# Kernel optimization log

Measured on AMD Instinct MI355X. Metric: run time of the kernel, lower is better.

## Reference

```python
import jax, jax.numpy as jnp
import numpy as np

N_NODES = 50000
N_EDGES = 800000
IN_C, HID_C, OUT_C = 256, 256, 128


def gcn_conv(x, W, b, row, col, n_nodes):
    """PyG GCNConv: linear transform, symmetric-normalized aggregation, bias.
    row/col already include self-loops. Messages flow row -> col."""
    h = x @ W  # [N, out]
    deg = jax.ops.segment_sum(jnp.ones_like(col, dtype=h.dtype), col, num_segments=n_nodes)
    d_inv_sqrt = jnp.where(deg > 0, jax.lax.rsqrt(jnp.maximum(deg, 1e-12)), 0.0)
    norm = d_inv_sqrt[row] * d_inv_sqrt[col]  # [E]
    msg = h[row] * norm[:, None]              # gather + scale, [E, out]
    out = jax.ops.segment_sum(msg, col, num_segments=n_nodes)  # scatter-add
    return out + b


def setup_inputs() -> dict:
    key = jax.random.key(0)
    k_x, k_e, k_w1, k_w2 = jax.random.split(key, 4)
    x = jax.random.normal(k_x, (N_NODES, IN_C), dtype=jnp.float32)
    edge_index = jax.random.randint(k_e, (2, N_EDGES), 0, N_NODES, dtype=jnp.int64)
    # Glorot-style init for GCN weights, zeros bias (PyG default)
    s1 = float(np.sqrt(6.0 / (IN_C + HID_C)))
    s2 = float(np.sqrt(6.0 / (HID_C + OUT_C)))
    W1 = jax.random.uniform(k_w1, (IN_C, HID_C), dtype=jnp.float32, minval=-s1, maxval=s1)
    b1 = jnp.zeros((HID_C,), dtype=jnp.float32)
    W2 = jax.random.uniform(k_w2, (HID_C, OUT_C), dtype=jnp.float32, minval=-s2, maxval=s2)
    b2 = jnp.zeros((OUT_C,), dtype=jnp.float32)
    return {"x": x, "edge_index": edge_index, "W1": W1, "b1": b1, "W2": W2, "b2": b2}


def reference(x, edge_index, W1, b1, W2, b2):
    n = x.shape[0]
    # add self-loops (PyG GCNConv default add_self_loops=True)
    loops = jnp.arange(n, dtype=edge_index.dtype)
    row = jnp.concatenate([edge_index[0], loops])
    col = jnp.concatenate([edge_index[1], loops])
    h = gcn_conv(x, W1, b1, row, col, n)
    h = jax.nn.relu(h)  # dropout p=0.0 -> identity
    out = gcn_conv(h, W2, b2, row, col, n)
    return out
```

## Files before the change

kernel.cpp:

```cpp
#include <hip/hip_runtime.h>

#define NN 50000
#define NE 800000
#define IN_C 256
#define HID_C 256
#define OUT_C 128

typedef unsigned short u16;
typedef __attribute__((ext_vector_type(8))) short short8;
typedef __attribute__((ext_vector_type(8))) unsigned short ushort8;
typedef __attribute__((ext_vector_type(4))) float f32x4;

__device__ __forceinline__ u16 f2b(float f) {
  unsigned int u = __float_as_uint(f);
  return (u16)((u + 0x7FFFu + ((u >> 16) & 1u)) >> 16);
}
__device__ __forceinline__ float b2f(u16 s) {
  return __uint_as_float(((unsigned int)s) << 16);
}


__global__ __launch_bounds__(256) void convw_zero(const float* __restrict__ W1,
                                                  const float* __restrict__ W2,
                                                  u16* __restrict__ W1t,
                                                  u16* __restrict__ W2t,
                                                  int* __restrict__ cnt) {
  int b = blockIdx.x;
  if (b < 256) {
    int id = b * 256 + threadIdx.x;
    if (id < 256 * 256) {
      int n = id >> 8, k = id & 255;
      W1t[id] = f2b(W1[k * 256 + n]);
    }
    if (id < 128 * 256) {
      int n = id >> 8, k = id & 255;
      W2t[id] = f2b(W2[k * 128 + n]);
    }
  } else {
    int i = (b - 256) * 256 + threadIdx.x;
    if (i < NN) cnt[i] = 0;
  }
}


__global__ __launch_bounds__(256) void hist_kernel(const int* __restrict__ col,
                                                   int* __restrict__ cnt, int E) {
  int e = blockIdx.x * blockDim.x + threadIdx.x;
  if (e < E) atomicAdd(&cnt[col[e]], 1);
}

__global__ __launch_bounds__(256) void scan1_kernel(const int* __restrict__ cnt,
                                                    int* __restrict__ bsum, int n) {
  __shared__ int ws[4];
  int i = blockIdx.x * 256 + threadIdx.x;
  int lane = threadIdx.x & 63, wid = threadIdx.x >> 6;
  int v = (i < n) ? cnt[i] : 0;
#pragma unroll
  for (int off = 32; off > 0; off >>= 1) v += __shfl_down(v, off, 64);
  if (lane == 0) ws[wid] = v;
  __syncthreads();
  if (threadIdx.x == 0) bsum[blockIdx.x] = ws[0] + ws[1] + ws[2] + ws[3];
}

__global__ __launch_bounds__(256) void scan2_kernel(const int* __restrict__ bsum,
                                                    int* __restrict__ boff,
                                                    int* __restrict__ row_off,
                                                    int nb, int n) {
  __shared__ int wsum[4], wpre[5];
  int lane = threadIdx.x & 63, wid = threadIdx.x >> 6;
  int v = (threadIdx.x < nb) ? bsum[threadIdx.x] : 0;
  int s = v;
#pragma unroll
  for (int off = 1; off < 64; off <<= 1) {
    int t = __shfl_up(s, off, 64);
    if (lane >= off) s += t;
  }
  if (lane == 63) wsum[wid] = s;
  __syncthreads();
  if (threadIdx.x == 0) {
    int acc = 0;
#pragma unroll
    for (int w = 0; w < 4; ++w) { wpre[w] = acc; acc += wsum[w]; }
    wpre[4] = acc;
  }
  __syncthreads();
  if (threadIdx.x < nb) boff[threadIdx.x] = wpre[wid] + (s - v);
  if (threadIdx.x == 0) row_off[n] = wpre[4];
}

__global__ __launch_bounds__(256) void scan3_kernel(const int* __restrict__ cnt,
                                                    const int* __restrict__ boff,
                                                    int* __restrict__ row_off,
                                                    int* __restrict__ cursor,
                                                    float* __restrict__ dinv, int n) {
  __shared__ int wsum[4], wpre[4];
  int i = blockIdx.x * 256 + threadIdx.x;
  int lane = threadIdx.x & 63, wid = threadIdx.x >> 6;
  int v = (i < n) ? cnt[i] : 0;
  int s = v;
#pragma unroll
  for (int off = 1; off < 64; off <<= 1) {
    int t = __shfl_up(s, off, 64);
    if (lane >= off) s += t;
  }
  if (lane == 63) wsum[wid] = s;
  __syncthreads();
  if (threadIdx.x == 0) {
    int acc = 0;
#pragma unroll
    for (int w = 0; w < 4; ++w) { wpre[w] = acc; acc += wsum[w]; }
  }
  __syncthreads();
  if (i < n) {
    int off = boff[blockIdx.x] + wpre[wid] + (s - v);
    row_off[i] = off;
    cursor[i] = off;
    dinv[i] = rsqrtf((float)(v + 1));
  }
}


template <bool A_IS_F32>
__device__ __forceinline__ void gemm_body(const void* __restrict__ Ap,
                                          const u16* __restrict__ Bt,
                                          const float* __restrict__ dscale,
                                          u16* __restrict__ C, int M, int N,
                                          int bx, int by,
                                          u16 (&Asl)[2][5120], u16 (&Bsl)[2][5120]) {
  const int tid = threadIdx.x;
  const int row0 = by * 128;
  const int col0 = bx * 128;

  f32x4 acc[4][4] = {};

  const int seg = tid & 7;
  const int rb = tid >> 3;
  const int wave = tid >> 6, lane = tid & 63;
  const int wm = wave >> 1, wn = wave & 1;
  const int qr = lane & 15, quad = lane >> 4;

  float4 aF[4];
  ushort4 aU[4];
  ushort4 bR[4];

  auto load_tiles = [&](int k0) {
    if constexpr (A_IS_F32) {
      const float* A = (const float*)Ap;
#pragma unroll
      for (int i = 0; i < 4; ++i) {
        int gr = row0 + rb + i * 32;
        aF[i] = (gr < M) ? *(const float4*)&A[(size_t)gr * 256 + k0 + seg * 4]
                         : make_float4(0.f, 0.f, 0.f, 0.f);
      }
    } else {
      const u16* A = (const u16*)Ap;
#pragma unroll
      for (int i = 0; i < 4; ++i) {
        int gr = row0 + rb + i * 32;
        aU[i] = (gr < M) ? *(const ushort4*)&A[(size_t)gr * 256 + k0 + seg * 4]
                         : make_ushort4(0, 0, 0, 0);
      }
    }
#pragma unroll
    for (int i = 0; i < 4; ++i) {
      int n = rb + i * 32;
      bR[i] = *(const ushort4*)&Bt[(size_t)(col0 + n) * 256 + k0 + seg * 4];
    }
  };

  auto write_lds = [&](int buf) {
#pragma unroll
    for (int i = 0; i < 4; ++i) {
      int r = rb + i * 32;
      ushort4 u;
      if constexpr (A_IS_F32) {
        u.x = f2b(aF[i].x); u.y = f2b(aF[i].y);
        u.z = f2b(aF[i].z); u.w = f2b(aF[i].w);
      } else {
        u = aU[i];
      }
      *(ushort4*)&Asl[buf][r * 40 + seg * 4] = u;
      *(ushort4*)&Bsl[buf][r * 40 + seg * 4] = bR[i];
    }
  };

  load_tiles(0);
  write_lds(0);
  __syncthreads();

#pragma unroll
  for (int it = 0; it < 8; ++it) {
    const int cur = it & 1;
    if (it < 7) load_tiles((it + 1) * 32);

    short8 afr[4], bfr[4];
#pragma unroll
    for (int mt = 0; mt < 4; ++mt)
      afr[mt] = *(const short8*)&Asl[cur][(wm * 64 + mt * 16 + qr) * 40 + quad * 8];
#pragma unroll
    for (int nt = 0; nt < 4; ++nt)
      bfr[nt] = *(const short8*)&Bsl[cur][(wn * 64 + nt * 16 + qr) * 40 + quad * 8];
#pragma unroll
    for (int mt = 0; mt < 4; ++mt)
#pragma unroll
      for (int nt = 0; nt < 4; ++nt)
        acc[mt][nt] = __builtin_amdgcn_mfma_f32_16x16x32_bf16(afr[mt], bfr[nt], acc[mt][nt], 0, 0, 0);

    if (it < 7) {
      write_lds(1 - cur);
      __syncthreads();
    }
  }

#pragma unroll
  for (int mt = 0; mt < 4; ++mt) {
#pragma unroll
    for (int i = 0; i < 4; ++i) {
      int gr = row0 + wm * 64 + mt * 16 + quad * 4 + i;
      if (gr < M) {
        float sc = dscale[gr];
#pragma unroll
        for (int nt = 0; nt < 4; ++nt) {
          int gc = col0 + wn * 64 + nt * 16 + qr;
          C[(size_t)gr * N + gc] = f2b(acc[mt][nt][i] * sc);
        }
      }
    }
  }
}

template <bool A_IS_F32>
__global__ __launch_bounds__(256) void gemm_mfma(const void* __restrict__ Ap,
                                                 const u16* __restrict__ Bt,
                                                 const float* __restrict__ dscale,
                                                 u16* __restrict__ C, int M, int N) {
  __shared__ u16 Asl[2][5120];
  __shared__ u16 Bsl[2][5120];
  gemm_body<A_IS_F32>(Ap, Bt, dscale, C, M, N, blockIdx.x, blockIdx.y, Asl, Bsl);
}

__global__ __launch_bounds__(256) void gemm1_scatter(const float* __restrict__ x,
                                                     const u16* __restrict__ W1t,
                                                     const float* __restrict__ dinv,
                                                     u16* __restrict__ Hb, int M, int N,
                                                     int ngb,
                                                     const int* __restrict__ row,
                                                     const int* __restrict__ col,
                                                     int* __restrict__ cursor,
                                                     int* __restrict__ csr, int E) {
  __shared__ u16 Asl[2][5120];
  __shared__ u16 Bsl[2][5120];
  int b = blockIdx.x;
  if (b < ngb) {
    gemm_body<true>(x, W1t, dinv, Hb, M, N, b & 1, b >> 1, Asl, Bsl);
  } else {
    int e = (b - ngb) * 256 + threadIdx.x;
    if (e < E) {
      int c = col[e];
      int p = atomicAdd(&cursor[c], 1);
      csr[p] = row[e];
    }
  }
}


__global__ __launch_bounds__(256) void agg256_bf(const u16* __restrict__ h,
                                                 const int* __restrict__ row_off,
                                                 const int* __restrict__ csr,
                                                 const float* __restrict__ dinv,
                                                 const float* __restrict__ bias,
                                                 u16* __restrict__ out, int n) {
  int wave = threadIdx.x >> 6;
  int lane = threadIdx.x & 63;
  int half = lane >> 5;
  int sl = lane & 31;
  int v = blockIdx.x * 8 + wave * 2 + half;
  if (v >= n) return;
  int beg = row_off[v], end = row_off[v + 1];
  float a[8] = {};
  int e = beg;
  for (; e < end && (e & 3); ++e) {
    int s0 = csr[e];
    ushort8 g0 = *(const ushort8*)&h[(size_t)s0 * 256 + sl * 8];
#pragma unroll
    for (int i = 0; i < 8; ++i) a[i] += b2f((u16)g0[i]);
  }
  for (; e + 7 < end; e += 8) {
    int4 i0 = *(const int4*)&csr[e];
    int4 i1 = *(const int4*)&csr[e + 4];
    int s[8] = {i0.x, i0.y, i0.z, i0.w, i1.x, i1.y, i1.z, i1.w};
    ushort8 g[8];
#pragma unroll
    for (int j = 0; j < 8; ++j)
      g[j] = *(const ushort8*)&h[(size_t)s[j] * 256 + sl * 8];
#pragma unroll
    for (int j = 0; j < 8; ++j)
#pragma unroll
      for (int i = 0; i < 8; ++i) a[i] += b2f((u16)g[j][i]);
  }
  for (; e < end; ++e) {
    int s0 = csr[e];
    ushort8 g0 = *(const ushort8*)&h[(size_t)s0 * 256 + sl * 8];
#pragma unroll
    for (int i = 0; i < 8; ++i) a[i] += b2f((u16)g0[i]);
  }
  ushort8 hs = *(const ushort8*)&h[(size_t)v * 256 + sl * 8];
#pragma unroll
  for (int i = 0; i < 8; ++i) a[i] += b2f((u16)hs[i]);
  float dv = dinv[v];
  float4 bv0 = *(const float4*)&bias[sl * 8];
  float4 bv1 = *(const float4*)&bias[sl * 8 + 4];
  float bb[8] = {bv0.x, bv0.y, bv0.z, bv0.w, bv1.x, bv1.y, bv1.z, bv1.w};
  ushort8 o;
#pragma unroll
  for (int i = 0; i < 8; ++i) {
    float r = fmaxf(a[i] * dv + bb[i], 0.f);
    o[i] = (short)f2b(r);
  }
  *(ushort8*)&out[(size_t)v * 256 + sl * 8] = o;
}

__global__ __launch_bounds__(256) void agg128_bf(const u16* __restrict__ h,
                                                 const int* __restrict__ row_off,
                                                 const int* __restrict__ csr,
                                                 const float* __restrict__ dinv,
                                                 const float* __restrict__ bias,
                                                 float* __restrict__ out, int n) {
  int wave = threadIdx.x >> 6;
  int lane = threadIdx.x & 63;
  int quarter = lane >> 4;
  int sl = lane & 15;
  int v = blockIdx.x * 16 + wave * 4 + quarter;
  if (v >= n) return;
  int beg = row_off[v], end = row_off[v + 1];
  float a[8] = {};
  int e = beg;
  for (; e < end && (e & 3); ++e) {
    int s0 = csr[e];
    ushort8 g0 = *(const ushort8*)&h[(size_t)s0 * 128 + sl * 8];
#pragma unroll
    for (int i = 0; i < 8; ++i) a[i] += b2f((u16)g0[i]);
  }
  for (; e + 7 < end; e += 8) {
    int4 i0 = *(const int4*)&csr[e];
    int4 i1 = *(const int4*)&csr[e + 4];
    int s[8] = {i0.x, i0.y, i0.z, i0.w, i1.x, i1.y, i1.z, i1.w};
    ushort8 g[8];
#pragma unroll
    for (int j = 0; j < 8; ++j)
      g[j] = *(const ushort8*)&h[(size_t)s[j] * 128 + sl * 8];
#pragma unroll
    for (int j = 0; j < 8; ++j)
#pragma unroll
      for (int i = 0; i < 8; ++i) a[i] += b2f((u16)g[j][i]);
  }
  for (; e < end; ++e) {
    int s0 = csr[e];
    ushort8 g0 = *(const ushort8*)&h[(size_t)s0 * 128 + sl * 8];
#pragma unroll
    for (int i = 0; i < 8; ++i) a[i] += b2f((u16)g0[i]);
  }
  ushort8 hs = *(const ushort8*)&h[(size_t)v * 128 + sl * 8];
#pragma unroll
  for (int i = 0; i < 8; ++i) a[i] += b2f((u16)hs[i]);
  float dv = dinv[v];
  float4 bv0 = *(const float4*)&bias[sl * 8];
  float4 bv1 = *(const float4*)&bias[sl * 8 + 4];
  float bb[8] = {bv0.x, bv0.y, bv0.z, bv0.w, bv1.x, bv1.y, bv1.z, bv1.w};
  float o[8];
#pragma unroll
  for (int i = 0; i < 8; ++i) o[i] = a[i] * dv + bb[i];
  *(float4*)&out[(size_t)v * 128 + sl * 8] = make_float4(o[0], o[1], o[2], o[3]);
  *(float4*)&out[(size_t)v * 128 + sl * 8 + 4] = make_float4(o[4], o[5], o[6], o[7]);
}


extern "C" void kernel_launch(void* const* d_in, const int* in_sizes, int n_in,
                              void* d_out, int out_size, void* d_ws, size_t ws_size,
                              hipStream_t stream) {
  const float* x = (const float*)d_in[0];
  const int* ei = (const int*)d_in[1];
  const float* W1 = (const float*)d_in[2];
  const float* b1 = (const float*)d_in[3];
  const float* W2 = (const float*)d_in[4];
  const float* b2 = (const float*)d_in[5];
  float* out = (float*)d_out;

  const int* row = ei;
  const int* col = ei + NE;

  const int NB = (NN + 255) / 256;

  u16* Hb = (u16*)d_ws;
  u16* H2b = Hb + (size_t)NN * 256;
  u16* H3b = H2b + (size_t)NN * 256;
  u16* W1t = H3b + (size_t)NN * 128;
  u16* W2t = W1t + 256 * 256;
  int* cnt = (int*)(W2t + 128 * 256);
  int* row_off = cnt + NN;
  int* cursor = row_off + NN + 4;
  float* dinv = (float*)(cursor + NN);
  int* bsum = (int*)(dinv + NN);
  int* boff = bsum + 200;
  int* csr = boff + 200;

  convw_zero<<<256 + NB, 256, 0, stream>>>(W1, W2, W1t, W2t, cnt);
  hist_kernel<<<(NE + 255) / 256, 256, 0, stream>>>(col, cnt, NE);
  scan1_kernel<<<NB, 256, 0, stream>>>(cnt, bsum, NN);
  scan2_kernel<<<1, 256, 0, stream>>>(bsum, boff, row_off, NB, NN);
  scan3_kernel<<<NB, 256, 0, stream>>>(cnt, boff, row_off, cursor, dinv, NN);

  {
    const int ngb = (HID_C / 128) * ((NN + 127) / 128);
    const int nsb = (NE + 255) / 256;
    gemm1_scatter<<<ngb + nsb, 256, 0, stream>>>(x, W1t, dinv, Hb, NN, HID_C, ngb,
                                                 row, col, cursor, csr, NE);
  }
  agg256_bf<<<(NN + 7) / 8, 256, 0, stream>>>(Hb, row_off, csr, dinv, b1, H2b, NN);

  {
    dim3 grid(OUT_C / 128, (NN + 127) / 128);
    gemm_mfma<false><<<grid, 256, 0, stream>>>(H2b, W2t, dinv, H3b, NN, OUT_C);
  }
  agg128_bf<<<(NN + 15) / 16, 256, 0, stream>>>(H3b, row_off, csr, dinv, b2, out, NN);
}
```

Before: 305.6 us.

## Build CSR via two-pass bucketed counting sort instead of global atomic scatter

Replaces the per-edge global atomicAdd on per-node cursors with a two-level counting sort. Edges are first binned by 256-node buckets in LDS and written out contiguously to a staging buffer, which reuses the H3b workspace. A new csr_sort kernel then places each bucket's edges into the CSR using shared-memory atomics and coalesced writes. This aims to cut global atomic contention and scattered writes, at the cost of one extra kernel launch and an extra pass over the edge data.

```diff
diff --git a/kernel.cpp b/kernel.cpp
--- a/kernel.cpp
+++ b/kernel.cpp
@@ -5,6 +5,11 @@
 #define IN_C 256
 #define HID_C 256
 #define OUT_C 128
+
+#define NBUCK 196
+#define CHUNK 4096
+#define NPA 196
+#define CAP_B 5120
 
 typedef unsigned short u16;
 typedef __attribute__((ext_vector_type(8))) short short8;
@@ -91,7 +96,7 @@
 __global__ __launch_bounds__(256) void scan3_kernel(const int* __restrict__ cnt,
                                                     const int* __restrict__ boff,
                                                     int* __restrict__ row_off,
-                                                    int* __restrict__ cursor,
+                                                    int* __restrict__ bcur,
                                                     float* __restrict__ dinv, int n) {
   __shared__ int wsum[4], wpre[4];
   int i = blockIdx.x * 256 + threadIdx.x;
@@ -114,7 +119,7 @@
   if (i < n) {
     int off = boff[blockIdx.x] + wpre[wid] + (s - v);
     row_off[i] = off;
-    cursor[i] = off;
+    if ((i & 255) == 0) bcur[i >> 8] = off;
     dinv[i] = rsqrtf((float)(v + 1));
   }
 }
@@ -246,21 +251,99 @@
                                                      int ngb,
                                                      const int* __restrict__ row,
                                                      const int* __restrict__ col,
-                                                     int* __restrict__ cursor,
-                                                     int* __restrict__ csr, int E) {
-  __shared__ u16 Asl[2][5120];
-  __shared__ u16 Bsl[2][5120];
+                                                     int* __restrict__ bcur,
+                                                     uint2* __restrict__ stage, int E) {
+  __shared__ u16 ABsl[4][5120];
   int b = blockIdx.x;
   if (b < ngb) {
-    gemm_body<true>(x, W1t, dinv, Hb, M, N, b & 1, b >> 1, Asl, Bsl);
+    gemm_body<true>(x, W1t, dinv, Hb, M, N, b & 1, b >> 1,
+                    *reinterpret_cast<u16(*)[2][5120]>(&ABsl[0]),
+                    *reinterpret_cast<u16(*)[2][5120]>(&ABsl[2]));
   } else {
-    int e = (b - ngb) * 256 + threadIdx.x;
-    if (e < E) {
-      int c = col[e];
-      int p = atomicAdd(&cursor[c], 1);
-      csr[p] = row[e];
-    }
-  }
+    uint2* pairs = (uint2*)ABsl;
+    int* hcnt = (int*)((char*)ABsl + 32768);
+    int* hscan = hcnt + 256;
+    int* hbase = hscan + 256;
+    int* lcur = hbase + 256;
+
+    const int tid = threadIdx.x;
+    const int blk = b - ngb;
+    const int e0 = blk * CHUNK;
+
+    hcnt[tid] = 0;
+    __syncthreads();
+
+    int ecol[16], erow[16];
+#pragma unroll
+    for (int j = 0; j < 16; ++j) {
+      int e = e0 + j * 256 + tid;
+      if (e < E) {
+        ecol[j] = col[e];
+        erow[j] = row[e];
+        atomicAdd(&hcnt[ecol[j] >> 8], 1);
+      } else {
+        ecol[j] = -1;
+      }
+    }
+    __syncthreads();
+
+    hscan[tid] = hcnt[tid];
+    __syncthreads();
+#pragma unroll
+    for (int off = 1; off < 256; off <<= 1) {
+      int t = (tid >= off) ? hscan[tid - off] : 0;
+      __syncthreads();
+      hscan[tid] += t;
+      __syncthreads();
+    }
+
+    lcur[tid] = 0;
+    if (hcnt[tid] > 0) hbase[tid] = atomicAdd(&bcur[tid], hcnt[tid]);
+    __syncthreads();
+
+#pragma unroll
+    for (int j = 0; j < 16; ++j) {
+      if (ecol[j] >= 0) {
+        int bk = ecol[j] >> 8;
+        int p = atomicAdd(&lcur[bk], 1);
+        pairs[(hscan[bk] - hcnt[bk]) + p] = make_uint2((unsigned)erow[j], (unsigned)ecol[j]);
+      }
+    }
+    __syncthreads();
+
+    int mtot = hscan[255];
+    for (int s = tid; s < mtot; s += 256) {
+      uint2 pr = pairs[s];
+      int bk = (int)(pr.y >> 8);
+      stage[hbase[bk] + (s - (hscan[bk] - hcnt[bk]))] = pr;
+    }
+  }
+}
+
+__global__ __launch_bounds__(256) void csr_sort(const uint2* __restrict__ stage,
+                                                const int* __restrict__ row_off,
+                                                int* __restrict__ csr) {
+  __shared__ int cur[256];
+  __shared__ int outb[CAP_B];
+  const int b = blockIdx.x;
+  const int base_node = b << 8;
+  const int nnodes = min(256, NN - base_node);
+  const int tid = threadIdx.x;
+  const int bstart = row_off[base_node];
+  const int bend = row_off[min(base_node + 256, NN)];
+  if (tid < nnodes) cur[tid] = row_off[base_node + tid] - bstart;
+  __syncthreads();
+  const int m = bend - bstart;
+  for (int i = tid; i < m; i += 256) {
+    uint2 pr = stage[bstart + i];
+    int cl = (int)pr.y - base_node;
+    int p = atomicAdd(&cur[cl], 1);
+    if (p < CAP_B) outb[p] = (int)pr.x;
+    else csr[bstart + p] = (int)pr.x;
+  }
+  __syncthreads();
+  const int mm = min(m, CAP_B);
+  for (int i = tid; i < mm; i += 256) csr[bstart + i] = outb[i];
 }
 
 
@@ -398,24 +481,25 @@
   u16* W2t = W1t + 256 * 256;
   int* cnt = (int*)(W2t + 128 * 256);
   int* row_off = cnt + NN;
-  int* cursor = row_off + NN + 4;
-  float* dinv = (float*)(cursor + NN);
+  int* bcur = row_off + NN + 4;
+  float* dinv = (float*)(bcur + 256);
   int* bsum = (int*)(dinv + NN);
   int* boff = bsum + 200;
   int* csr = boff + 200;
+  uint2* stage = (uint2*)H3b;
 
   convw_zero<<<256 + NB, 256, 0, stream>>>(W1, W2, W1t, W2t, cnt);
   hist_kernel<<<(NE + 255) / 256, 256, 0, stream>>>(col, cnt, NE);
   scan1_kernel<<<NB, 256, 0, stream>>>(cnt, bsum, NN);
   scan2_kernel<<<1, 256, 0, stream>>>(bsum, boff, row_off, NB, NN);
-  scan3_kernel<<<NB, 256, 0, stream>>>(cnt, boff, row_off, cursor, dinv, NN);
+  scan3_kernel<<<NB, 256, 0, stream>>>(cnt, boff, row_off, bcur, dinv, NN);
 
   {
     const int ngb = (HID_C / 128) * ((NN + 127) / 128);
-    const int nsb = (NE + 255) / 256;
-    gemm1_scatter<<<ngb + nsb, 256, 0, stream>>>(x, W1t, dinv, Hb, NN, HID_C, ngb,
-                                                 row, col, cursor, csr, NE);
-  }
+    gemm1_scatter<<<ngb + NPA, 256, 0, stream>>>(x, W1t, dinv, Hb, NN, HID_C, ngb,
+                                                 row, col, bcur, stage, NE);
+  }
+  csr_sort<<<NBUCK, 256, 0, stream>>>(stage, row_off, csr);
   agg256_bf<<<(NN + 7) / 8, 256, 0, stream>>>(Hb, row_off, csr, dinv, b1, H2b, NN);
 
   {
```

Measured after the change: 293.4 us. -4.0%, faster.
